# Kernel optimization log

Hardware: AMD Instinct MI355X
Metric: run time of the kernel (lower is better)

Reference implementation:

```python
import jax, jax.numpy as jnp
import numpy as np

SCALE = 8
MAX_DEPTH = 81.0
PI = 3.1415926535


def setup_inputs() -> dict:
    key = jax.random.key(0)
    ks = jax.random.split(key, 13)
    B, C, H8, W8 = 16, 128, 44, 144
    d = {"x": jax.random.normal(ks[0], (B, C, H8, W8), jnp.float32)}
    chans = [128, 64, 32, 16, 8, 4]  # reduction chain of 1x1 convs
    for i in range(5):
        d[f"w{i}"] = jax.random.normal(ks[1 + 2 * i], (chans[i + 1], chans[i]), jnp.float32) * 0.05
        d[f"b{i}"] = jnp.zeros((chans[i + 1],), jnp.float32)
    d["wc"] = jax.random.normal(ks[11], (3, 4), jnp.float32) * 0.05  # final 4->3 1x1 conv
    d["bc"] = jnp.zeros((3,), jnp.float32)
    return d


def _conv1x1(x, w, b):
    # x: [B,C,H,W], w: [O,C] -> [B,O,H,W]
    return jnp.einsum('bchw,oc->bohw', x, w) + b[None, :, None, None]


def reference(x, w0, b0, w1, b1, w2, b2, w3, b3, w4, b4, wc, bc):
    elu = jax.nn.elu
    h = elu(_conv1x1(x, w0, b0))
    h = elu(_conv1x1(h, w1, b1))
    h = elu(_conv1x1(h, w2, b2))
    h = elu(_conv1x1(h, w3, b3))
    h = _conv1x1(h, w4, b4)          # [B,4,H8,W8], no activation on last reduction
    y = _conv1x1(h, wc, bc)          # [B,3,H8,W8]

    theta = jax.nn.sigmoid(y[:, 0]) * PI / 6.0
    phi = jax.nn.sigmoid(y[:, 1]) * PI * 2.0
    dist = jax.nn.sigmoid(y[:, 2]) * MAX_DEPTH

    st = jnp.sin(theta)
    n = jnp.stack([st * jnp.cos(phi), st * jnp.sin(phi), jnp.cos(theta)], axis=1)  # [B,3,H8,W8]
    # F.normalize(p=2, dim=1, eps=1e-12)
    norm = jnp.maximum(jnp.sqrt(jnp.sum(n * n, axis=1, keepdims=True)), 1e-12)
    n = n / norm
    plane = jnp.concatenate([n, dist[:, None]], axis=1)  # [B,4,H8,W8]

    # repeat_interleave upsample by SCALE on H then W
    pe = jnp.repeat(jnp.repeat(plane, SCALE, axis=2), SCALE, axis=3)  # [B,4,H,W]
    B, _, H, W = pe.shape

    # local-plane coordinate grids (tiled arange pattern per torch.Tensor.repeat)
    u = (jnp.tile(jnp.arange(SCALE, dtype=jnp.float32), W // SCALE) - (SCALE - 1) * 0.5) / SCALE  # [W]
    v = (jnp.tile(jnp.arange(SCALE, dtype=jnp.float32), H // SCALE) - (SCALE - 1) * 0.5) / SCALE  # [H]

    depth = pe[:, 3] / (pe[:, 0] * u[None, None, :] + pe[:, 1] * v[None, :, None] + pe[:, 2])
    return depth[:, None]  # [B,1,H,W]
```

## Files before the change

### kernel.cpp

```cpp
#include <hip/hip_runtime.h>

#define NB   16
#define C0   128
#define HH   44
#define WW   144
#define HW   (HH * WW)
#define NPOS (NB * HW)
#define SC   8
#define WOUT (WW * SC)
#define HOUT (HH * SC)
#define PI_F 3.1415926535f

typedef __attribute__((ext_vector_type(8))) short bf8;
typedef __attribute__((ext_vector_type(4))) float f4;

__device__ __forceinline__ unsigned short f2bf(float f) {
    union { float f; unsigned u; } v; v.f = f;
    unsigned r = v.u + 0x7FFFu + ((v.u >> 16) & 1u);
    return (unsigned short)(r >> 16);
}
__device__ __forceinline__ float eluf(float x) {
    return x > 0.f ? x : (__expf(x) - 1.f);
}
__device__ __forceinline__ float sigmoidf(float x) {
    return 1.f / (1.f + __expf(-x));
}

#define W0B 0
#define W1B 8704
#define W2B 11008
#define WSM_N 11648
#define H1B 0
#define H2B 1152
#define H3F 1792

__global__ __launch_bounds__(256, 3)
void lpg_mfma(const float* __restrict__ x,
              const float* __restrict__ w0, const float* __restrict__ b0,
              const float* __restrict__ w1, const float* __restrict__ b1,
              const float* __restrict__ w2, const float* __restrict__ b2,
              const float* __restrict__ w3, const float* __restrict__ b3,
              const float* __restrict__ w4, const float* __restrict__ b4,
              const float* __restrict__ wc, const float* __restrict__ bc,
              float* __restrict__ out) {
    __shared__ __align__(16) unsigned short wsm[WSM_N];
    __shared__ __align__(16) unsigned short hbuf[4][2432];

    const int tid  = (int)threadIdx.x;
    const int lane = tid & 63;
    const int wid  = tid >> 6;
    const int q    = lane >> 4;
    const int n    = lane & 15;

    const int p0 = blockIdx.x * 64 + wid * 16;
    const int pm = p0 + n;
    const int bm = pm / HW;
    const int hwm = pm - bm * HW;

    const float* xb = x + (size_t)bm * (C0 * HW) + hwm;
    float xr[32];
#pragma unroll
    for (int kk = 0; kk < 4; ++kk)
#pragma unroll
        for (int j = 0; j < 8; ++j)
            xr[kk * 8 + j] = xb[(kk * 32 + q * 8 + j) * HW];

#pragma unroll
    for (int k = 0; k < 32; ++k) { int i = tid + 256 * k; int o = i >> 7, c = i & 127; wsm[W0B + o * 136 + c] = f2bf(w0[i]); }
#pragma unroll
    for (int k = 0; k < 8; ++k)  { int i = tid + 256 * k; int o = i >> 6, c = i & 63;  wsm[W1B + o * 72  + c] = f2bf(w1[i]); }
#pragma unroll
    for (int k = 0; k < 2; ++k)  { int i = tid + 256 * k; int o = i >> 5, c = i & 31;  wsm[W2B + o * 40  + c] = f2bf(w2[i]); }
    __syncthreads();

    bf8 A[4];
#pragma unroll
    for (int kk = 0; kk < 4; ++kk) {
        bf8 a;
#pragma unroll
        for (int j = 0; j < 8; ++j) a[j] = (short)f2bf(xr[kk * 8 + j]);
        A[kk] = a;
    }

    f4 acc[4];
#pragma unroll
    for (int t = 0; t < 4; ++t) acc[t] = (f4){0.f, 0.f, 0.f, 0.f};
#pragma unroll
    for (int t = 0; t < 4; ++t) {
        bf8 B[4];
#pragma unroll
        for (int kk = 0; kk < 4; ++kk)
            B[kk] = *(const bf8*)(wsm + W0B + (t * 16 + n) * 136 + kk * 32 + q * 8);
#pragma unroll
        for (int kk = 0; kk < 4; ++kk)
            acc[t] = __builtin_amdgcn_mfma_f32_16x16x32_bf16(A[kk], B[kk], acc[t], 0, 0, 0);
    }

    unsigned short* hb = &hbuf[wid][0];
#pragma unroll
    for (int t = 0; t < 4; ++t) {
        const float bb = b0[t * 16 + n];
#pragma unroll
        for (int r = 0; r < 4; ++r)
            hb[H1B + (q * 4 + r) * 72 + t * 16 + n] = f2bf(eluf(acc[t][r] + bb));
    }

    bf8 A1[2];
#pragma unroll
    for (int kk = 0; kk < 2; ++kk)
        A1[kk] = *(const bf8*)(hb + H1B + n * 72 + kk * 32 + q * 8);
    f4 acc1[2];
#pragma unroll
    for (int t = 0; t < 2; ++t) acc1[t] = (f4){0.f, 0.f, 0.f, 0.f};
#pragma unroll
    for (int t = 0; t < 2; ++t)
#pragma unroll
        for (int kk = 0; kk < 2; ++kk) {
            bf8 B = *(const bf8*)(wsm + W1B + (t * 16 + n) * 72 + kk * 32 + q * 8);
            acc1[t] = __builtin_amdgcn_mfma_f32_16x16x32_bf16(A1[kk], B, acc1[t], 0, 0, 0);
        }
#pragma unroll
    for (int t = 0; t < 2; ++t) {
        const float bb = b1[t * 16 + n];
#pragma unroll
        for (int r = 0; r < 4; ++r)
            hb[H2B + (q * 4 + r) * 40 + t * 16 + n] = f2bf(eluf(acc1[t][r] + bb));
    }

    bf8 A2 = *(const bf8*)(hb + H2B + n * 40 + q * 8);
    bf8 B2 = *(const bf8*)(wsm + W2B + n * 40 + q * 8);
    f4 acc2 = (f4){0.f, 0.f, 0.f, 0.f};
    acc2 = __builtin_amdgcn_mfma_f32_16x16x32_bf16(A2, B2, acc2, 0, 0, 0);
    float* h3f = (float*)(hb + H3F);
    {
        const float bb = b2[n];
#pragma unroll
        for (int r = 0; r < 4; ++r)
            h3f[(q * 4 + r) * 20 + n] = eluf(acc2[r] + bb);
    }

    float h3[16];
#pragma unroll
    for (int i = 0; i < 4; ++i) {
        f4 v = *(const f4*)(h3f + n * 20 + i * 4);
        h3[4 * i + 0] = v[0]; h3[4 * i + 1] = v[1];
        h3[4 * i + 2] = v[2]; h3[4 * i + 3] = v[3];
    }

    float h4v[8];
#pragma unroll
    for (int o = 0; o < 8; ++o) {
        float a = b3[o];
#pragma unroll
        for (int c = 0; c < 16; ++c) a = fmaf(h3[c], w3[o * 16 + c], a);
        h4v[o] = eluf(a);
    }
    float h5v[4];
#pragma unroll
    for (int o = 0; o < 4; ++o) {
        float a = b4[o];
#pragma unroll
        for (int c = 0; c < 8; ++c) a = fmaf(h4v[c], w4[o * 8 + c], a);
        h5v[o] = a;
    }
    float y0 = bc[0], y1 = bc[1], y2 = bc[2];
#pragma unroll
    for (int c = 0; c < 4; ++c) {
        y0 = fmaf(h5v[c], wc[0 * 4 + c], y0);
        y1 = fmaf(h5v[c], wc[1 * 4 + c], y1);
        y2 = fmaf(h5v[c], wc[2 * 4 + c], y2);
    }

    const float theta = sigmoidf(y0) * (PI_F / 6.0f);
    const float phi   = sigmoidf(y1) * (PI_F * 2.0f);
    const float dist  = sigmoidf(y2) * 81.0f;
    const float st = __sinf(theta), ct = __cosf(theta);
    const float sp = __sinf(phi),   cp = __cosf(phi);
    float nx = st * cp, ny = st * sp, nz = ct;
    const float inv = rsqrtf(fmaxf(nx * nx + ny * ny + nz * nz, 1e-24f));
    nx *= inv; ny *= inv; nz *= inv;

    const int hh = hwm / WW;
    const int wp = hwm - hh * WW;
    float* op = out + ((size_t)bm * HOUT + (size_t)hh * SC) * WOUT + (size_t)wp * SC;

    float nxu[8];
#pragma unroll
    for (int j = 0; j < 8; ++j) nxu[j] = nx * ((j - 3.5f) * 0.125f);

#pragma unroll
    for (int ii = 0; ii < 2; ++ii) {
        const int i = q * 2 + ii;
        const float den0 = fmaf(ny, (i - 3.5f) * 0.125f, nz);
        float d[8];
#pragma unroll
        for (int j = 0; j < 8; ++j)
            d[j] = dist * __builtin_amdgcn_rcpf(den0 + nxu[j]);
        float* row = op + (size_t)i * WOUT;
        *reinterpret_cast<float4*>(row)     = make_float4(d[0], d[1], d[2], d[3]);
        *reinterpret_cast<float4*>(row + 4) = make_float4(d[4], d[5], d[6], d[7]);
    }
}

extern "C" void kernel_launch(void* const* d_in, const int* in_sizes, int n_in,
                              void* d_out, int out_size, void* d_ws, size_t ws_size,
                              hipStream_t stream) {
    const float* x  = (const float*)d_in[0];
    const float* w0 = (const float*)d_in[1];  const float* b0 = (const float*)d_in[2];
    const float* w1 = (const float*)d_in[3];  const float* b1 = (const float*)d_in[4];
    const float* w2 = (const float*)d_in[5];  const float* b2 = (const float*)d_in[6];
    const float* w3 = (const float*)d_in[7];  const float* b3 = (const float*)d_in[8];
    const float* w4 = (const float*)d_in[9];  const float* b4 = (const float*)d_in[10];
    const float* wc = (const float*)d_in[11]; const float* bc = (const float*)d_in[12];
    float* out = (float*)d_out;

    hipLaunchKernelGGL(lpg_mfma, dim3(NPOS / 64), dim3(256), 0, stream,
                       x, w0, b0, w1, b1, w2, b2, w3, b3, w4, b4, wc, bc, out);
}
```

Measured before the change: 123.6 us.

## Pre-pack bf16 weights in MFMA fragment order via prep kernel, drop LDS staging

A small prep kernel converts w0/w1/w2 to bf16 once per call and stores them in workspace in per-lane MFMA fragment order. The main kernel then reads B fragments straight from global/L2 as contiguous 16-byte loads, which removes the per-block LDS weight staging, its conversions and the __syncthreads. Biases are folded into the accumulator init, x is converted with packed bf16 conversion, and launch bounds rise to 4 blocks per CU. The cost is an extra kernel launch and global weight reads on every block, which rely on L2/L1 hits.

```diff
diff --git a/kernel.cpp b/kernel.cpp
--- a/kernel.cpp
+++ b/kernel.cpp
@@ -1,4 +1,5 @@
 #include <hip/hip_runtime.h>
+#include <hip/hip_bf16.h>
 
 #define NB   16
 #define C0   128
@@ -13,6 +14,12 @@
 
 typedef __attribute__((ext_vector_type(8))) short bf8;
 typedef __attribute__((ext_vector_type(4))) float f4;
+typedef unsigned short ushort_t;
+
+#define F0 0
+#define F1 8192
+#define F2 10240
+#define NWT 10752
 
 __device__ __forceinline__ unsigned short f2bf(float f) {
     union { float f; unsigned u; } v; v.f = f;
@@ -26,25 +33,39 @@
     return 1.f / (1.f + __expf(-x));
 }
 
-#define W0B 0
-#define W1B 8704
-#define W2B 11008
-#define WSM_N 11648
+__global__ void prep_w(const float* __restrict__ w0, const float* __restrict__ w1,
+                       const float* __restrict__ w2, ushort_t* __restrict__ ws) {
+    int i = blockIdx.x * 256 + (int)threadIdx.x;
+    if (i < 8192) {
+        int j = i & 7, lane = (i >> 3) & 63, ch = i >> 9;
+        int q = lane >> 4, n = lane & 15, kk = ch & 3, t = ch >> 2;
+        ws[F0 + i] = f2bf(w0[(t * 16 + n) * 128 + kk * 32 + q * 8 + j]);
+    } else if (i < 10240) {
+        int i2 = i - 8192;
+        int j = i2 & 7, lane = (i2 >> 3) & 63, ch = i2 >> 9;
+        int q = lane >> 4, n = lane & 15, kk = ch & 1, t = ch >> 1;
+        ws[F1 + i2] = f2bf(w1[(t * 16 + n) * 64 + kk * 32 + q * 8 + j]);
+    } else if (i < NWT) {
+        int i2 = i - 10240;
+        int j = i2 & 7, lane = (i2 >> 3) & 63;
+        int q = lane >> 4, n = lane & 15;
+        ws[F2 + i2] = f2bf(w2[n * 32 + q * 8 + j]);
+    }
+}
+
 #define H1B 0
 #define H2B 1152
 #define H3F 1792
 
-__global__ __launch_bounds__(256, 3)
-void lpg_mfma(const float* __restrict__ x,
-              const float* __restrict__ w0, const float* __restrict__ b0,
-              const float* __restrict__ w1, const float* __restrict__ b1,
-              const float* __restrict__ w2, const float* __restrict__ b2,
-              const float* __restrict__ w3, const float* __restrict__ b3,
-              const float* __restrict__ w4, const float* __restrict__ b4,
+__global__ __launch_bounds__(256, 4)
+void lpg_mfma(const float* __restrict__ x, const ushort_t* __restrict__ wsb,
+              const float* __restrict__ b0, const float* __restrict__ b1,
+              const float* __restrict__ b2, const float* __restrict__ b3,
+              const float* __restrict__ w3, const float* __restrict__ w4,
+              const float* __restrict__ b4,
               const float* __restrict__ wc, const float* __restrict__ bc,
               float* __restrict__ out) {
-    __shared__ __align__(16) unsigned short wsm[WSM_N];
-    __shared__ __align__(16) unsigned short hbuf[4][2432];
+    __shared__ __align__(16) ushort_t hbuf[4][2432];
 
     const int tid  = (int)threadIdx.x;
     const int lane = tid & 63;
@@ -52,8 +73,7 @@
     const int q    = lane >> 4;
     const int n    = lane & 15;
 
-    const int p0 = blockIdx.x * 64 + wid * 16;
-    const int pm = p0 + n;
+    const int pm = blockIdx.x * 64 + wid * 16 + n;
     const int bm = pm / HW;
     const int hwm = pm - bm * HW;
 
@@ -65,45 +85,43 @@
         for (int j = 0; j < 8; ++j)
             xr[kk * 8 + j] = xb[(kk * 32 + q * 8 + j) * HW];
 
-#pragma unroll
-    for (int k = 0; k < 32; ++k) { int i = tid + 256 * k; int o = i >> 7, c = i & 127; wsm[W0B + o * 136 + c] = f2bf(w0[i]); }
-#pragma unroll
-    for (int k = 0; k < 8; ++k)  { int i = tid + 256 * k; int o = i >> 6, c = i & 63;  wsm[W1B + o * 72  + c] = f2bf(w1[i]); }
-#pragma unroll
-    for (int k = 0; k < 2; ++k)  { int i = tid + 256 * k; int o = i >> 5, c = i & 31;  wsm[W2B + o * 40  + c] = f2bf(w2[i]); }
-    __syncthreads();
-
     bf8 A[4];
 #pragma unroll
     for (int kk = 0; kk < 4; ++kk) {
         bf8 a;
 #pragma unroll
-        for (int j = 0; j < 8; ++j) a[j] = (short)f2bf(xr[kk * 8 + j]);
+        for (int j = 0; j < 8; j += 2) {
+            __hip_bfloat162 p = __float22bfloat162_rn(
+                make_float2(xr[kk * 8 + j], xr[kk * 8 + j + 1]));
+            union { __hip_bfloat162 b; short s[2]; } u; u.b = p;
+            a[j] = u.s[0]; a[j + 1] = u.s[1];
+        }
         A[kk] = a;
     }
 
     f4 acc[4];
 #pragma unroll
-    for (int t = 0; t < 4; ++t) acc[t] = (f4){0.f, 0.f, 0.f, 0.f};
+    for (int t = 0; t < 4; ++t) {
+        const float bb = b0[t * 16 + n];
+        acc[t] = (f4){bb, bb, bb, bb};
+    }
 #pragma unroll
     for (int t = 0; t < 4; ++t) {
         bf8 B[4];
 #pragma unroll
         for (int kk = 0; kk < 4; ++kk)
-            B[kk] = *(const bf8*)(wsm + W0B + (t * 16 + n) * 136 + kk * 32 + q * 8);
+            B[kk] = *(const bf8*)(wsb + F0 + (t * 4 + kk) * 512 + lane * 8);
 #pragma unroll
         for (int kk = 0; kk < 4; ++kk)
             acc[t] = __builtin_amdgcn_mfma_f32_16x16x32_bf16(A[kk], B[kk], acc[t], 0, 0, 0);
     }
 
-    unsigned short* hb = &hbuf[wid][0];
-#pragma unroll
-    for (int t = 0; t < 4; ++t) {
-        const float bb = b0[t * 16 + n];
+    ushort_t* hb = &hbuf[wid][0];
+#pragma unroll
+    for (int t = 0; t < 4; ++t)
 #pragma unroll
         for (int r = 0; r < 4; ++r)
-            hb[H1B + (q * 4 + r) * 72 + t * 16 + n] = f2bf(eluf(acc[t][r] + bb));
-    }
+            hb[H1B + (q * 4 + r) * 72 + t * 16 + n] = f2bf(eluf(acc[t][r]));
 
     bf8 A1[2];
 #pragma unroll
@@ -111,33 +129,32 @@
         A1[kk] = *(const bf8*)(hb + H1B + n * 72 + kk * 32 + q * 8);
     f4 acc1[2];
 #pragma unroll
-    for (int t = 0; t < 2; ++t) acc1[t] = (f4){0.f, 0.f, 0.f, 0.f};
+    for (int t = 0; t < 2; ++t) {
+        const float bb = b1[t * 16 + n];
+        acc1[t] = (f4){bb, bb, bb, bb};
+    }
 #pragma unroll
     for (int t = 0; t < 2; ++t)
 #pragma unroll
         for (int kk = 0; kk < 2; ++kk) {
-            bf8 B = *(const bf8*)(wsm + W1B + (t * 16 + n) * 72 + kk * 32 + q * 8);
+            bf8 B = *(const bf8*)(wsb + F1 + (t * 2 + kk) * 512 + lane * 8);
             acc1[t] = __builtin_amdgcn_mfma_f32_16x16x32_bf16(A1[kk], B, acc1[t], 0, 0, 0);
         }
 #pragma unroll
-    for (int t = 0; t < 2; ++t) {
-        const float bb = b1[t * 16 + n];
+    for (int t = 0; t < 2; ++t)
 #pragma unroll
         for (int r = 0; r < 4; ++r)
-            hb[H2B + (q * 4 + r) * 40 + t * 16 + n] = f2bf(eluf(acc1[t][r] + bb));
-    }
+            hb[H2B + (q * 4 + r) * 40 + t * 16 + n] = f2bf(eluf(acc1[t][r]));
 
     bf8 A2 = *(const bf8*)(hb + H2B + n * 40 + q * 8);
-    bf8 B2 = *(const bf8*)(wsm + W2B + n * 40 + q * 8);
-    f4 acc2 = (f4){0.f, 0.f, 0.f, 0.f};
+    bf8 B2 = *(const bf8*)(wsb + F2 + lane * 8);
+    const float bb2 = b2[n];
+    f4 acc2 = (f4){bb2, bb2, bb2, bb2};
     acc2 = __builtin_amdgcn_mfma_f32_16x16x32_bf16(A2, B2, acc2, 0, 0, 0);
     float* h3f = (float*)(hb + H3F);
-    {
-        const float bb = b2[n];
-#pragma unroll
-        for (int r = 0; r < 4; ++r)
-            h3f[(q * 4 + r) * 20 + n] = eluf(acc2[r] + bb);
-    }
+#pragma unroll
+    for (int r = 0; r < 4; ++r)
+        h3f[(q * 4 + r) * 20 + n] = eluf(acc2[r]);
 
     float h3[16];
 #pragma unroll
@@ -212,8 +229,11 @@
     const float* w3 = (const float*)d_in[7];  const float* b3 = (const float*)d_in[8];
     const float* w4 = (const float*)d_in[9];  const float* b4 = (const float*)d_in[10];
     const float* wc = (const float*)d_in[11]; const float* bc = (const float*)d_in[12];
+    ushort_t* ws = (ushort_t*)d_ws;
     float* out = (float*)d_out;
 
+    hipLaunchKernelGGL(prep_w, dim3((NWT + 255) / 256), dim3(256), 0, stream,
+                       w0, w1, w2, ws);
     hipLaunchKernelGGL(lpg_mfma, dim3(NPOS / 64), dim3(256), 0, stream,
-                       x, w0, b0, w1, b1, w2, b2, w3, b3, w4, b4, wc, bc, out);
-}
+                       x, ws, b0, b1, b2, b3, w3, w4, b4, wc, bc, out);
+}
```

New measurement: 122.6 us. No clear change (-0.9%).
